# Kernel optimization log

Hardware: AMD Instinct MI355X
Metric: run time of the kernel (lower is better)

Reference implementation:

```python
import jax, jax.numpy as jnp
import numpy as np

B = 512      # batch (len(missing_type))
HALF = 12    # prompt_length // 3
D = 12       # prompt_depth
DT = 512     # text embed dim
DI = 768     # image embed dim
E = DT + DI  # 1280, concat dim
R = 16
H = E // R    # 80
HC = DT // R  # 32
EPS = 1e-5


def _ln(x, g, b):
    m = jnp.mean(x, -1, keepdims=True)
    v = jnp.mean((x - m) ** 2, -1, keepdims=True)
    return (x - m) * jax.lax.rsqrt(v + EPS) * g + b


def _mlp(x, w1, b1, w2, b2):
    return jax.nn.gelu(x @ w1 + b1, approximate=False) @ w2 + b2


def setup_inputs() -> dict:
    key = jax.random.key(0)
    ks = jax.random.split(key, 20)
    n = lambda k, s: jax.random.normal(k, s, dtype=jnp.float32) * 0.02
    return {
        "missing_type": jax.random.randint(ks[0], (B,), 0, 3),
        "vpc": n(ks[1], (HALF, DI)), "vpm": n(ks[2], (HALF, DI)),
        "tpc": n(ks[3], (HALF, DT)), "tpm": n(ks[4], (HALF, DT)),
        "cpc": n(ks[5], (HALF, DT)), "cpi": n(ks[6], (HALF, DT)), "cpt": n(ks[7], (HALF, DT)),
        "ln_img_g": jnp.ones((D, E)), "ln_img_b": jnp.zeros((D, E)),
        "ln_txt_g": jnp.ones((D, E)), "ln_txt_b": jnp.zeros((D, E)),
        "img_w1": n(ks[8], (D, E, H)), "img_b1": jnp.zeros((D, H)),
        "img_w2": n(ks[9], (D, H, DI)), "img_b2": jnp.zeros((D, DI)),
        "txt_w1": n(ks[10], (D, E, H)), "txt_b1": jnp.zeros((D, H)),
        "txt_w2": n(ks[11], (D, H, DT)), "txt_b2": jnp.zeros((D, DT)),
        "cimg_w1": n(ks[12], (DT, HC)), "cimg_b1": jnp.zeros((HC,)),
        "cimg_w2": n(ks[13], (HC, DI)), "cimg_b2": jnp.zeros((DI,)),
        "ctxt_w1": n(ks[14], (DT, HC)), "ctxt_b1": jnp.zeros((HC,)),
        "ctxt_w2": n(ks[15], (HC, DT)), "ctxt_b2": jnp.zeros((DT,)),
    }


def reference(missing_type, vpc, vpm, tpc, tpm, cpc, cpi, cpt,
              ln_img_g, ln_img_b, ln_txt_g, ln_txt_b,
              img_w1, img_b1, img_w2, img_b2,
              txt_w1, txt_b1, txt_w2, txt_b2,
              cimg_w1, cimg_b1, cimg_w2, cimg_b2,
              ctxt_w1, ctxt_b1, ctxt_w2, ctxt_b2):
    depth = img_w1.shape[0]
    mt = missing_type
    # per-sample branch selection, vectorized over the batch
    img = jnp.where((mt == 2)[:, None, None], vpm[None], vpc[None])  # [B,HALF,768]
    txt = jnp.where((mt == 1)[:, None, None], tpm[None], tpc[None])  # [B,HALF,512]
    common = jnp.stack([cpc, cpi, cpt])[mt]                          # [B,HALF,512]
    imgs, txts = [], []
    for d in range(depth):  # sequential depth dependency
        x = jnp.concatenate([img, txt], -1)  # [B,HALF,1280]
        img = _mlp(_ln(x, ln_img_g[d], ln_img_b[d]), img_w1[d], img_b1[d], img_w2[d], img_b2[d])
        txt = _mlp(_ln(x, ln_txt_g[d], ln_txt_b[d]), txt_w1[d], txt_b1[d], txt_w2[d], txt_b2[d])
        imgs.append(img)
        txts.append(txt)
    # depth-0 prompts get the projected common prompt appended along tokens
    img0 = jnp.concatenate([imgs[0], _mlp(common, cimg_w1, cimg_b1, cimg_w2, cimg_b2)], axis=1)
    txt0 = jnp.concatenate([txts[0], _mlp(common, ctxt_w1, ctxt_b1, ctxt_w2, ctxt_b2)], axis=1)
    return (img0, txt0, jnp.stack(imgs[1:]), jnp.stack(txts[1:]))
```

## Files before the change

kernel.cpp:

```cpp
#include <hip/hip_runtime.h>

typedef unsigned int u32;
typedef unsigned short u16;

#define TPB 640

namespace {
constexpr size_t F_WP1  = 0;
constexpr size_t F_WP2  = 1228800;
constexpr size_t F_XI_P = 1843200;
constexpr size_t F_XT_P = 2174976;
constexpr size_t F_CI_P = 2396160;
constexpr size_t F_CT_P = 2423808;
constexpr size_t F_END_P = 2442240;
constexpr size_t F_XI_U = 0;
constexpr size_t F_XT_U = 331776;
constexpr size_t F_CI_U = 552960;
constexpr size_t F_CT_U = 580608;
}

__device__ __forceinline__ float bflo(u32 u) { return __uint_as_float(u << 16); }
__device__ __forceinline__ float bfhi(u32 u) { return __uint_as_float(u & 0xffff0000u); }
__device__ __forceinline__ float gelu_f(float x) { return 0.5f * x * (1.0f + erff(x * 0.70710678118654752f)); }
__device__ __forceinline__ u16 f2bf(float f) {
    u32 u = __float_as_uint(f);
    u += 0x7fffu + ((u >> 16) & 1u);
    return (u16)(u >> 16);
}

struct P {
    const float *vpc, *vpm, *tpc, *tpm, *cpc, *cpi, *cpt;
    const float *lig, *lib, *ltg, *ltb;
    const float *iw1, *ib1, *iw2, *ib2;
    const float *tw1, *tb1, *tw2, *tb2;
    const float *ciw1, *cib1, *ciw2, *cib2;
    const float *ctw1, *ctb1, *ctw2, *ctb2;
    const u16 *wp1, *wp2;
    float *xi, *xt, *cimg, *ctxt;
};

__global__ __launch_bounds__(256) void prep_kernel(P p, u32* wp1o, u32* wp2o) {
    constexpr u32 N1 = 12u * 1280 * 80;
    constexpr u32 N2 = 12u * 80 * 640;
    u32 i = blockIdx.x * 256 + threadIdx.x;
    if (i < N1) {
        u32 j2 = i % 80, rem = i / 80;
        u32 k = rem % 1280, d = rem / 1280;
        u32 j0 = 2 * j2;
        const float* s = (j0 < 80) ? (p.iw1 + ((size_t)(d * 1280) + k) * 80 + j0)
                                   : (p.tw1 + ((size_t)(d * 1280) + k) * 80 + (j0 - 80));
        float2 v = *reinterpret_cast<const float2*>(s);
        wp1o[i] = (u32)f2bf(v.x) | ((u32)f2bf(v.y) << 16);
    } else {
        u32 ii = i - N1;
        if (ii >= N2) return;
        u32 c2 = ii % 640, rem = ii / 640;
        u32 k = rem % 80, d = rem / 80;
        u32 c0 = 2 * c2;
        const float* s = (c0 < 768) ? (p.iw2 + ((size_t)(d * 80) + k) * 768 + c0)
                                    : (p.tw2 + ((size_t)(d * 80) + k) * 512 + (c0 - 768));
        float2 v = *reinterpret_cast<const float2*>(s);
        wp2o[ii] = (u32)f2bf(v.x) | ((u32)f2bf(v.y) << 16);
    }
}

template <int PACKED>
__global__ __launch_bounds__(TPB) void chain_kernel(P p) {
    __shared__ float smem[6592];
    float* sx   = smem;
    float* xln0 = smem + 1280;
    float* xln1 = smem + 2560;
    float* part = smem + 3840;
    float* hh   = smem + 6400;
    float* redA = smem + 6560;
    float* redB = smem + 6570;
    float* st   = smem + 6580;

    const int tid = threadIdx.x;
    const int blk = blockIdx.x;

    if (blk < 36) {
        const int v = blk / 12, t = blk % 12;
        const float* is = (v == 2) ? p.vpm : p.vpc;
        const float* ts = (v == 1) ? p.tpm : p.tpc;
        if (tid < 512) { sx[768 + tid] = ts[t * 512 + tid]; }
        for (int k = tid; k < 768; k += TPB) sx[k] = is[t * 768 + k];
        __syncthreads();

        for (int d = 0; d < 12; ++d) {
            {
                float x0 = sx[tid], x1 = sx[tid + 640];
                float s = x0 + x1, s2 = x0 * x0 + x1 * x1;
                #pragma unroll
                for (int off = 32; off > 0; off >>= 1) { s += __shfl_down(s, off); s2 += __shfl_down(s2, off); }
                if ((tid & 63) == 0) { redA[tid >> 6] = s; redB[tid >> 6] = s2; }
            }
            __syncthreads();
            if (tid == 0) {
                float S = 0.f, S2 = 0.f;
                #pragma unroll
                for (int w = 0; w < 10; ++w) { S += redA[w]; S2 += redB[w]; }
                float m = S * (1.0f / 1280.0f);
                float var = S2 * (1.0f / 1280.0f) - m * m;
                st[0] = m; st[1] = rsqrtf(var + 1e-5f);
            }
            __syncthreads();
            const float m = st[0], rs = st[1];
            #pragma unroll
            for (int q = 0; q < 2; ++q) {
                const int k = tid + 640 * q;
                float xc = (sx[k] - m) * rs;
                xln0[k] = xc * p.lig[d * 1280 + k] + p.lib[d * 1280 + k];
                xln1[k] = xc * p.ltg[d * 1280 + k] + p.ltb[d * 1280 + k];
            }
            __syncthreads();
            {
                const int g = tid % 40, kc = tid / 40;
                const int j0 = 4 * g;
                const float* xl = (j0 >= 80) ? xln1 : xln0;
                const int k0 = kc * 80;
                float a0 = 0.f, a1 = 0.f, a2 = 0.f, a3 = 0.f;
                if (PACKED) {
                    const u16* wp = p.wp1 + ((size_t)(d * 1280) + k0) * 160 + j0;
                    #pragma unroll 16
                    for (int i = 0; i < 80; ++i) {
                        uint2 w = *reinterpret_cast<const uint2*>(wp);
                        float xv = xl[k0 + i];
                        a0 += xv * bflo(w.x); a1 += xv * bfhi(w.x);
                        a2 += xv * bflo(w.y); a3 += xv * bfhi(w.y);
                        wp += 160;
                    }
                } else {
                    const float* wp = (j0 < 80) ? (p.iw1 + ((size_t)(d * 1280) + k0) * 80 + j0)
                                                : (p.tw1 + ((size_t)(d * 1280) + k0) * 80 + (j0 - 80));
                    #pragma unroll 8
                    for (int i = 0; i < 80; ++i) {
                        float4 w = *reinterpret_cast<const float4*>(wp);
                        float xv = xl[k0 + i];
                        a0 += xv * w.x; a1 += xv * w.y; a2 += xv * w.z; a3 += xv * w.w;
                        wp += 80;
                    }
                }
                *reinterpret_cast<float4*>(part + kc * 160 + j0) = make_float4(a0, a1, a2, a3);
            }
            __syncthreads();
            if (tid < 160) {
                const int path = tid >= 80, j = tid - 80 * path;
                float a = (path ? p.tb1 : p.ib1)[d * 80 + j];
                #pragma unroll
                for (int kc = 0; kc < 16; ++kc) a += part[kc * 160 + tid];
                hh[tid] = gelu_f(a);
            }
            __syncthreads();
            {
                const int c = tid;
                const int pth = (c >= 384);
                const int cc = 2 * c - 768 * pth;
                const float* hb = hh + 80 * pth;
                float a0, a1;
                {
                    const float* b2 = (pth ? p.tb2 : p.ib2) + d * (pth ? 512 : 768) + cc;
                    a0 = b2[0]; a1 = b2[1];
                }
                if (PACKED) {
                    const u16* wp = p.wp2 + (size_t)(d * 80) * 1280 + 2 * c;
                    #pragma unroll 16
                    for (int k = 0; k < 80; ++k) {
                        u32 w = *reinterpret_cast<const u32*>(wp);
                        float hv = hb[k];
                        a0 += hv * bflo(w); a1 += hv * bfhi(w);
                        wp += 1280;
                    }
                } else {
                    const int Np = pth ? 512 : 768;
                    const float* wp = (pth ? p.tw2 + (size_t)(d * 80) * 512 : p.iw2 + (size_t)(d * 80) * 768) + cc;
                    #pragma unroll 16
                    for (int k = 0; k < 80; ++k) {
                        float2 w = *reinterpret_cast<const float2*>(wp);
                        float hv = hb[k];
                        a0 += hv * w.x; a1 += hv * w.y;
                        wp += Np;
                    }
                }
                sx[2 * c] = a0; sx[2 * c + 1] = a1;
                float* xo = pth ? (p.xt + ((size_t)(d * 36) + blk) * 512 + cc)
                                : (p.xi + ((size_t)(d * 36) + blk) * 768 + cc);
                *reinterpret_cast<float2*>(xo) = make_float2(a0, a1);
            }
            __syncthreads();
        }
    } else {
        float* cx  = smem;
        float* ph  = smem + 512;
        float* hhl = smem + 768;
        const int rr = blk - 36, v = rr / 12, t = rr % 12;
        const float* cs = (v == 0) ? p.cpc : (v == 1) ? p.cpi : p.cpt;
        if (tid < 512) cx[tid] = cs[t * 512 + tid];
        __syncthreads();
        if (tid < 256) {
            const int o = tid & 63, kc = tid >> 6;
            const int path = o >> 5, j = o & 31;
            const float* w = (path ? p.ctw1 : p.ciw1) + (size_t)(kc * 128) * 32 + j;
            float a = 0.f;
            #pragma unroll 8
            for (int i = 0; i < 128; ++i) { a += cx[kc * 128 + i] * (*w); w += 32; }
            ph[kc * 64 + o] = a;
        }
        __syncthreads();
        if (tid < 64) {
            const int path = tid >> 5, j = tid & 31;
            float a = (path ? p.ctb1 : p.cib1)[j];
            #pragma unroll
            for (int kc = 0; kc < 4; ++kc) a += ph[kc * 64 + tid];
            hhl[tid] = gelu_f(a);
        }
        __syncthreads();
        for (int o = tid; o < 1280; o += TPB) {
            if (o < 768) {
                float a = p.cib2[o];
                #pragma unroll
                for (int k = 0; k < 32; ++k) a += hhl[k] * p.ciw2[k * 768 + o];
                p.cimg[rr * 768 + o] = a;
            } else {
                const int oo = o - 768;
                float a = p.ctb2[oo];
                #pragma unroll
                for (int k = 0; k < 32; ++k) a += hhl[32 + k] * p.ctw2[k * 512 + oo];
                p.ctxt[rr * 512 + oo] = a;
            }
        }
    }
}

__global__ __launch_bounds__(256) void emit_kernel(const int* __restrict__ mt,
                                                   const float* __restrict__ xi,
                                                   const float* __restrict__ xt,
                                                   const float* __restrict__ cimg,
                                                   const float* __restrict__ ctxt,
                                                   float* __restrict__ out) {
    constexpr unsigned int C0 = 512u * 24 * 192;
    constexpr unsigned int C1 = 512u * 24 * 128;
    constexpr unsigned int C2 = 11u * 512 * 12 * 192;
    constexpr unsigned int C3 = 11u * 512 * 12 * 128;
    constexpr unsigned int TOT = C0 + C1 + C2 + C3;
    const unsigned int stride = gridDim.x * blockDim.x;
    for (unsigned int c = blockIdx.x * blockDim.x + threadIdx.x; c < TOT; c += stride) {
        const float* src;
        if (c < C0) {
            unsigned int b = c / 4608u, r = c % 4608u;
            unsigned int tok = r / 192u, col = (r % 192u) * 4u;
            int v = mt[b];
            src = (tok < 12u) ? xi + ((size_t)v * 12 + tok) * 768 + col
                              : cimg + ((size_t)v * 12 + (tok - 12u)) * 768 + col;
        } else if (c < C0 + C1) {
            unsigned int cc = c - C0;
            unsigned int b = cc / 3072u, r = cc % 3072u;
            unsigned int tok = r / 128u, col = (r % 128u) * 4u;
            int v = mt[b];
            src = (tok < 12u) ? xt + ((size_t)v * 12 + tok) * 512 + col
                              : ctxt + ((size_t)v * 12 + (tok - 12u)) * 512 + col;
        } else if (c < C0 + C1 + C2) {
            unsigned int cc = c - C0 - C1;
            unsigned int d = cc / 1179648u, r = cc % 1179648u;
            unsigned int b = r / 2304u, rr = r % 2304u;
            unsigned int tok = rr / 192u, col = (rr % 192u) * 4u;
            int v = mt[b];
            src = xi + ((size_t)(d + 1) * 36 + v * 12 + tok) * 768 + col;
        } else {
            unsigned int cc = c - C0 - C1 - C2;
            unsigned int d = cc / 786432u, r = cc % 786432u;
            unsigned int b = r / 1536u, rr = r % 1536u;
            unsigned int tok = rr / 128u, col = (rr % 128u) * 4u;
            int v = mt[b];
            src = xt + ((size_t)(d + 1) * 36 + v * 12 + tok) * 512 + col;
        }
        *reinterpret_cast<float4*>(out + (size_t)c * 4) = *reinterpret_cast<const float4*>(src);
    }
}

extern "C" void kernel_launch(void* const* d_in, const int* in_sizes, int n_in,
                              void* d_out, int out_size, void* d_ws, size_t ws_size,
                              hipStream_t stream) {
    const int* mt = (const int*)d_in[0];
    float* ws = (float*)d_ws;
    P p;
    p.vpc  = (const float*)d_in[1];
    p.vpm  = (const float*)d_in[2];
    p.tpc  = (const float*)d_in[3];
    p.tpm  = (const float*)d_in[4];
    p.cpc  = (const float*)d_in[5];
    p.cpi  = (const float*)d_in[6];
    p.cpt  = (const float*)d_in[7];
    p.lig  = (const float*)d_in[8];
    p.lib  = (const float*)d_in[9];
    p.ltg  = (const float*)d_in[10];
    p.ltb  = (const float*)d_in[11];
    p.iw1  = (const float*)d_in[12];
    p.ib1  = (const float*)d_in[13];
    p.iw2  = (const float*)d_in[14];
    p.ib2  = (const float*)d_in[15];
    p.tw1  = (const float*)d_in[16];
    p.tb1  = (const float*)d_in[17];
    p.tw2  = (const float*)d_in[18];
    p.tb2  = (const float*)d_in[19];
    p.ciw1 = (const float*)d_in[20];
    p.cib1 = (const float*)d_in[21];
    p.ciw2 = (const float*)d_in[22];
    p.cib2 = (const float*)d_in[23];
    p.ctw1 = (const float*)d_in[24];
    p.ctb1 = (const float*)d_in[25];
    p.ctw2 = (const float*)d_in[26];
    p.ctb2 = (const float*)d_in[27];

    const bool packed = (ws_size >= F_END_P * sizeof(float));
    if (packed) {
        p.wp1  = (const u16*)(ws + F_WP1);
        p.wp2  = (const u16*)(ws + F_WP2);
        p.xi   = ws + F_XI_P;
        p.xt   = ws + F_XT_P;
        p.cimg = ws + F_CI_P;
        p.ctxt = ws + F_CT_P;
        constexpr u32 NPAIR = 12u * 1280 * 80 + 12u * 80 * 640;
        prep_kernel<<<dim3((NPAIR + 255) / 256), dim3(256), 0, stream>>>(p, (u32*)(ws + F_WP1), (u32*)(ws + F_WP2));
        chain_kernel<1><<<dim3(72), dim3(TPB), 0, stream>>>(p);
    } else {
        p.wp1 = nullptr; p.wp2 = nullptr;
        p.xi   = ws + F_XI_U;
        p.xt   = ws + F_XT_U;
        p.cimg = ws + F_CI_U;
        p.ctxt = ws + F_CT_U;
        chain_kernel<0><<<dim3(72), dim3(TPB), 0, stream>>>(p);
    }
    emit_kernel<<<dim3(4096), dim3(256), 0, stream>>>(mt, p.xi, p.xt, p.cimg, p.ctxt, (float*)d_out);
}
```

Before: 216.1 us.

## Fold LayerNorm affine into packed first-layer weights and split K for second GEMV

The prep kernel now folds the LayerNorm gamma into the bf16 first-layer weights and precomputes per-column sums (s1) and bias-folded offsets (t1). The chain kernel can then run the first GEMV directly on the raw activations and apply mean and rstd afterwards, which removes the normalized-activation pass and one barrier. The first GEMV now reads 8 outputs per thread with wider loads, and the second GEMV is split over two K-chunks so all 640 threads work on it. The cost is an extra reduction step and a slower prep kernel that loops serially over K. The algebraic rewrite can also lose precision when the mean is large.

```diff
diff --git a/kernel.cpp b/kernel.cpp
--- a/kernel.cpp
+++ b/kernel.cpp
@@ -8,11 +8,13 @@
 namespace {
 constexpr size_t F_WP1  = 0;
 constexpr size_t F_WP2  = 1228800;
-constexpr size_t F_XI_P = 1843200;
-constexpr size_t F_XT_P = 2174976;
-constexpr size_t F_CI_P = 2396160;
-constexpr size_t F_CT_P = 2423808;
-constexpr size_t F_END_P = 2442240;
+constexpr size_t F_S1   = 1843200;
+constexpr size_t F_T1   = 1845120;
+constexpr size_t F_XI_P = 1847040;
+constexpr size_t F_XT_P = 2178816;
+constexpr size_t F_CI_P = 2400000;
+constexpr size_t F_CT_P = 2427648;
+constexpr size_t F_END_P = 2446080;
 constexpr size_t F_XI_U = 0;
 constexpr size_t F_XT_U = 331776;
 constexpr size_t F_CI_U = 552960;
@@ -36,36 +38,191 @@
     const float *ciw1, *cib1, *ciw2, *cib2;
     const float *ctw1, *ctb1, *ctw2, *ctb2;
     const u16 *wp1, *wp2;
+    const float *s1, *t1;
     float *xi, *xt, *cimg, *ctxt;
 };
 
-__global__ __launch_bounds__(256) void prep_kernel(P p, u32* wp1o, u32* wp2o) {
-    constexpr u32 N1 = 12u * 1280 * 80;
-    constexpr u32 N2 = 12u * 80 * 640;
-    u32 i = blockIdx.x * 256 + threadIdx.x;
-    if (i < N1) {
-        u32 j2 = i % 80, rem = i / 80;
-        u32 k = rem % 1280, d = rem / 1280;
-        u32 j0 = 2 * j2;
-        const float* s = (j0 < 80) ? (p.iw1 + ((size_t)(d * 1280) + k) * 80 + j0)
-                                   : (p.tw1 + ((size_t)(d * 1280) + k) * 80 + (j0 - 80));
-        float2 v = *reinterpret_cast<const float2*>(s);
-        wp1o[i] = (u32)f2bf(v.x) | ((u32)f2bf(v.y) << 16);
+__global__ __launch_bounds__(320) void prep_kernel(P p, u16* wp1o, u32* wp2o, float* s1o, float* t1o) {
+    __shared__ float sA[4][80], sB[4][80];
+    const int t = threadIdx.x;
+    if (blockIdx.x < 24) {
+        const int d = blockIdx.x >> 1, path = blockIdx.x & 1;
+        const float* W1 = (path ? p.tw1 : p.iw1) + (size_t)d * 1280 * 80;
+        const float* G  = (path ? p.ltg : p.lig) + d * 1280;
+        const float* Bb = (path ? p.ltb : p.lib) + d * 1280;
+        const int j = t % 80, kc = t / 80;
+        float S = 0.f, T = 0.f;
+        for (int k = kc * 320; k < kc * 320 + 320; ++k) {
+            float w = W1[(size_t)k * 80 + j];
+            float wg = G[k] * w;
+            S += wg; T += Bb[k] * w;
+            wp1o[((size_t)(d * 1280) + k) * 160 + path * 80 + j] = f2bf(wg);
+        }
+        sA[kc][j] = S; sB[kc][j] = T;
+        __syncthreads();
+        if (t < 80) {
+            float Ssum = sA[0][t] + sA[1][t] + sA[2][t] + sA[3][t];
+            float Tsum = sB[0][t] + sB[1][t] + sB[2][t] + sB[3][t];
+            s1o[d * 160 + path * 80 + t] = Ssum;
+            t1o[d * 160 + path * 80 + t] = Tsum + (path ? p.tb1 : p.ib1)[d * 80 + t];
+        }
     } else {
-        u32 ii = i - N1;
-        if (ii >= N2) return;
-        u32 c2 = ii % 640, rem = ii / 640;
+        constexpr u32 N2 = 12u * 80 * 640;
+        u32 i = (blockIdx.x - 24) * 320 + t;
+        if (i >= N2) return;
+        u32 c2 = i % 640, rem = i / 640;
         u32 k = rem % 80, d = rem / 80;
         u32 c0 = 2 * c2;
         const float* s = (c0 < 768) ? (p.iw2 + ((size_t)(d * 80) + k) * 768 + c0)
                                     : (p.tw2 + ((size_t)(d * 80) + k) * 512 + (c0 - 768));
         float2 v = *reinterpret_cast<const float2*>(s);
-        wp2o[ii] = (u32)f2bf(v.x) | ((u32)f2bf(v.y) << 16);
+        wp2o[i] = (u32)f2bf(v.x) | ((u32)f2bf(v.y) << 16);
     }
 }
 
-template <int PACKED>
-__global__ __launch_bounds__(TPB) void chain_kernel(P p) {
+__global__ __launch_bounds__(TPB) void chain2_kernel(P p) {
+    __shared__ float smem[6608];
+    float* sx   = smem;
+    float* part = smem + 1280;
+    float* hh   = smem + 6400;
+    float* redA = smem + 6560;
+    float* redB = smem + 6580;
+    float* st   = smem + 6600;
+
+    const int tid = threadIdx.x;
+    const int blk = blockIdx.x;
+
+    if (blk < 36) {
+        const int v = blk / 12, t = blk % 12;
+        const float* is = (v == 2) ? p.vpm : p.vpc;
+        const float* ts = (v == 1) ? p.tpm : p.tpc;
+        for (int k = tid; k < 768; k += TPB) sx[k] = is[t * 768 + k];
+        if (tid < 512) sx[768 + tid] = ts[t * 512 + tid];
+        __syncthreads();
+
+        for (int d = 0; d < 12; ++d) {
+            {
+                float x0 = sx[tid], x1 = sx[tid + 640];
+                float s = x0 + x1, s2 = x0 * x0 + x1 * x1;
+                #pragma unroll
+                for (int off = 32; off > 0; off >>= 1) { s += __shfl_down(s, off); s2 += __shfl_down(s2, off); }
+                if ((tid & 63) == 0) { redA[tid >> 6] = s; redB[tid >> 6] = s2; }
+            }
+            __syncthreads();
+            if (tid == 0) {
+                float S = 0.f, S2 = 0.f;
+                #pragma unroll
+                for (int w = 0; w < 10; ++w) { S += redA[w]; S2 += redB[w]; }
+                float m = S * (1.0f / 1280.0f);
+                float var = S2 * (1.0f / 1280.0f) - m * m;
+                st[0] = m; st[1] = rsqrtf(var + 1e-5f);
+            }
+            {
+                const int g = tid % 20, kc = tid / 20;
+                const int j0 = 8 * g, k0 = 40 * kc;
+                const u16* wp = p.wp1 + ((size_t)(d * 1280) + k0) * 160 + j0;
+                float a0 = 0.f, a1 = 0.f, a2 = 0.f, a3 = 0.f;
+                float a4 = 0.f, a5 = 0.f, a6 = 0.f, a7 = 0.f;
+                #pragma unroll 8
+                for (int i = 0; i < 40; ++i) {
+                    uint4 w = *reinterpret_cast<const uint4*>(wp);
+                    float xv = sx[k0 + i];
+                    a0 += xv * bflo(w.x); a1 += xv * bfhi(w.x);
+                    a2 += xv * bflo(w.y); a3 += xv * bfhi(w.y);
+                    a4 += xv * bflo(w.z); a5 += xv * bfhi(w.z);
+                    a6 += xv * bflo(w.w); a7 += xv * bfhi(w.w);
+                    wp += 160;
+                }
+                *reinterpret_cast<float4*>(part + kc * 160 + j0)     = make_float4(a0, a1, a2, a3);
+                *reinterpret_cast<float4*>(part + kc * 160 + j0 + 4) = make_float4(a4, a5, a6, a7);
+            }
+            __syncthreads();
+            if (tid < 160) {
+                float y = 0.f;
+                #pragma unroll
+                for (int kc = 0; kc < 32; ++kc) y += part[kc * 160 + tid];
+                const float m = st[0], rs = st[1];
+                float hpre = rs * y - m * rs * p.s1[d * 160 + tid] + p.t1[d * 160 + tid];
+                hh[tid] = gelu_f(hpre);
+            }
+            __syncthreads();
+            {
+                const int g2 = tid % 320, kc = tid / 320;
+                const int c0 = 4 * g2, k0 = 40 * kc;
+                const u16* wq = p.wp2 + ((size_t)(d * 80) + k0) * 1280 + c0;
+                const float* hb = hh + ((c0 >= 768) ? 80 : 0);
+                float a0 = 0.f, a1 = 0.f, a2 = 0.f, a3 = 0.f;
+                #pragma unroll 8
+                for (int i = 0; i < 40; ++i) {
+                    uint2 w = *reinterpret_cast<const uint2*>(wq);
+                    float hv = hb[k0 + i];
+                    a0 += hv * bflo(w.x); a1 += hv * bfhi(w.x);
+                    a2 += hv * bflo(w.y); a3 += hv * bfhi(w.y);
+                    wq += 1280;
+                }
+                *reinterpret_cast<float4*>(part + kc * 1280 + c0) = make_float4(a0, a1, a2, a3);
+            }
+            __syncthreads();
+            {
+                const int c0 = 2 * tid;
+                const int pth = (c0 >= 768);
+                const int cc = c0 - 768 * pth;
+                const int Np = pth ? 512 : 768;
+                float2 bb = *reinterpret_cast<const float2*>((pth ? p.tb2 : p.ib2) + d * Np + cc);
+                float a0 = part[c0]     + part[1280 + c0]     + bb.x;
+                float a1 = part[c0 + 1] + part[1280 + c0 + 1] + bb.y;
+                __syncthreads();
+                sx[c0] = a0; sx[c0 + 1] = a1;
+                float* xo = pth ? (p.xt + ((size_t)(d * 36) + blk) * 512 + cc)
+                                : (p.xi + ((size_t)(d * 36) + blk) * 768 + cc);
+                *reinterpret_cast<float2*>(xo) = make_float2(a0, a1);
+            }
+            __syncthreads();
+        }
+    } else {
+        float* cx  = smem;
+        float* ph  = smem + 512;
+        float* hhl = smem + 768;
+        const int rr = blk - 36, v = rr / 12, t = rr % 12;
+        const float* cs = (v == 0) ? p.cpc : (v == 1) ? p.cpi : p.cpt;
+        if (tid < 512) cx[tid] = cs[t * 512 + tid];
+        __syncthreads();
+        if (tid < 256) {
+            const int o = tid & 63, kc = tid >> 6;
+            const int path = o >> 5, j = o & 31;
+            const float* w = (path ? p.ctw1 : p.ciw1) + (size_t)(kc * 128) * 32 + j;
+            float a = 0.f;
+            #pragma unroll 8
+            for (int i = 0; i < 128; ++i) { a += cx[kc * 128 + i] * (*w); w += 32; }
+            ph[kc * 64 + o] = a;
+        }
+        __syncthreads();
+        if (tid < 64) {
+            const int path = tid >> 5, j = tid & 31;
+            float a = (path ? p.ctb1 : p.cib1)[j];
+            #pragma unroll
+            for (int kc = 0; kc < 4; ++kc) a += ph[kc * 64 + tid];
+            hhl[tid] = gelu_f(a);
+        }
+        __syncthreads();
+        for (int o = tid; o < 1280; o += TPB) {
+            if (o < 768) {
+                float a = p.cib2[o];
+                #pragma unroll
+                for (int k = 0; k < 32; ++k) a += hhl[k] * p.ciw2[k * 768 + o];
+                p.cimg[rr * 768 + o] = a;
+            } else {
+                const int oo = o - 768;
+                float a = p.ctb2[oo];
+                #pragma unroll
+                for (int k = 0; k < 32; ++k) a += hhl[32 + k] * p.ctw2[k * 512 + oo];
+                p.ctxt[rr * 512 + oo] = a;
+            }
+        }
+    }
+}
+
+__global__ __launch_bounds__(TPB) void chain_fb_kernel(P p) {
     __shared__ float smem[6592];
     float* sx   = smem;
     float* xln0 = smem + 1280;
@@ -83,10 +240,9 @@
         const int v = blk / 12, t = blk % 12;
         const float* is = (v == 2) ? p.vpm : p.vpc;
         const float* ts = (v == 1) ? p.tpm : p.tpc;
-        if (tid < 512) { sx[768 + tid] = ts[t * 512 + tid]; }
+        if (tid < 512) sx[768 + tid] = ts[t * 512 + tid];
         for (int k = tid; k < 768; k += TPB) sx[k] = is[t * 768 + k];
         __syncthreads();
-
         for (int d = 0; d < 12; ++d) {
             {
                 float x0 = sx[tid], x1 = sx[tid + 640];
@@ -120,26 +276,14 @@
                 const float* xl = (j0 >= 80) ? xln1 : xln0;
                 const int k0 = kc * 80;
                 float a0 = 0.f, a1 = 0.f, a2 = 0.f, a3 = 0.f;
-                if (PACKED) {
-                    const u16* wp = p.wp1 + ((size_t)(d * 1280) + k0) * 160 + j0;
-                    #pragma unroll 16
-                    for (int i = 0; i < 80; ++i) {
-                        uint2 w = *reinterpret_cast<const uint2*>(wp);
-                        float xv = xl[k0 + i];
-                        a0 += xv * bflo(w.x); a1 += xv * bfhi(w.x);
-                        a2 += xv * bflo(w.y); a3 += xv * bfhi(w.y);
-                        wp += 160;
-                    }
-                } else {
-                    const float* wp = (j0 < 80) ? (p.iw1 + ((size_t)(d * 1280) + k0) * 80 + j0)
-                                                : (p.tw1 + ((size_t)(d * 1280) + k0) * 80 + (j0 - 80));
-                    #pragma unroll 8
-                    for (int i = 0; i < 80; ++i) {
-                        float4 w = *reinterpret_cast<const float4*>(wp);
-                        float xv = xl[k0 + i];
-                        a0 += xv * w.x; a1 += xv * w.y; a2 += xv * w.z; a3 += xv * w.w;
-                        wp += 80;
-                    }
+                const float* wp = (j0 < 80) ? (p.iw1 + ((size_t)(d * 1280) + k0) * 80 + j0)
+                                            : (p.tw1 + ((size_t)(d * 1280) + k0) * 80 + (j0 - 80));
+                #pragma unroll 8
+                for (int i = 0; i < 80; ++i) {
+                    float4 w = *reinterpret_cast<const float4*>(wp);
+                    float xv = xl[k0 + i];
+                    a0 += xv * w.x; a1 += xv * w.y; a2 += xv * w.z; a3 += xv * w.w;
+                    wp += 80;
                 }
                 *reinterpret_cast<float4*>(part + kc * 160 + j0) = make_float4(a0, a1, a2, a3);
             }
@@ -157,30 +301,16 @@
                 const int pth = (c >= 384);
                 const int cc = 2 * c - 768 * pth;
                 const float* hb = hh + 80 * pth;
-                float a0, a1;
-                {
-                    const float* b2 = (pth ? p.tb2 : p.ib2) + d * (pth ? 512 : 768) + cc;
-                    a0 = b2[0]; a1 = b2[1];
-                }
-                if (PACKED) {
-                    const u16* wp = p.wp2 + (size_t)(d * 80) * 1280 + 2 * c;
-                    #pragma unroll 16
-                    for (int k = 0; k < 80; ++k) {
-                        u32 w = *reinterpret_cast<const u32*>(wp);
-                        float hv = hb[k];
-                        a0 += hv * bflo(w); a1 += hv * bfhi(w);
-                        wp += 1280;
-                    }
-                } else {
-                    const int Np = pth ? 512 : 768;
-                    const float* wp = (pth ? p.tw2 + (size_t)(d * 80) * 512 : p.iw2 + (size_t)(d * 80) * 768) + cc;
-                    #pragma unroll 16
-                    for (int k = 0; k < 80; ++k) {
-                        float2 w = *reinterpret_cast<const float2*>(wp);
-                        float hv = hb[k];
-                        a0 += hv * w.x; a1 += hv * w.y;
-                        wp += Np;
-                    }
+                const int Np = pth ? 512 : 768;
+                const float* b2 = (pth ? p.tb2 : p.ib2) + d * Np + cc;
+                float a0 = b2[0], a1 = b2[1];
+                const float* wp = (pth ? p.tw2 + (size_t)(d * 80) * 512 : p.iw2 + (size_t)(d * 80) * 768) + cc;
+                #pragma unroll 16
+                for (int k = 0; k < 80; ++k) {
+                    float2 w = *reinterpret_cast<const float2*>(wp);
+                    float hv = hb[k];
+                    a0 += hv * w.x; a1 += hv * w.y;
+                    wp += Np;
                 }
                 sx[2 * c] = a0; sx[2 * c + 1] = a1;
                 float* xo = pth ? (p.xt + ((size_t)(d * 36) + blk) * 512 + cc)
@@ -316,20 +446,24 @@
     if (packed) {
         p.wp1  = (const u16*)(ws + F_WP1);
         p.wp2  = (const u16*)(ws + F_WP2);
+        p.s1   = ws + F_S1;
+        p.t1   = ws + F_T1;
         p.xi   = ws + F_XI_P;
         p.xt   = ws + F_XT_P;
         p.cimg = ws + F_CI_P;
         p.ctxt = ws + F_CT_P;
-        constexpr u32 NPAIR = 12u * 1280 * 80 + 12u * 80 * 640;
-        prep_kernel<<<dim3((NPAIR + 255) / 256), dim3(256), 0, stream>>>(p, (u32*)(ws + F_WP1), (u32*)(ws + F_WP2));
-        chain_kernel<1><<<dim3(72), dim3(TPB), 0, stream>>>(p);
+        constexpr u32 N2 = 12u * 80 * 640;
+        const int nb = 24 + (N2 + 319) / 320;
+        prep_kernel<<<dim3(nb), dim3(320), 0, stream>>>(p, (u16*)(ws + F_WP1), (u32*)(ws + F_WP2),
+                                                        ws + F_S1, ws + F_T1);
+        chain2_kernel<<<dim3(72), dim3(TPB), 0, stream>>>(p);
     } else {
-        p.wp1 = nullptr; p.wp2 = nullptr;
+        p.wp1 = nullptr; p.wp2 = nullptr; p.s1 = nullptr; p.t1 = nullptr;
         p.xi   = ws + F_XI_U;
         p.xt   = ws + F_XT_U;
         p.cimg = ws + F_CI_U;
         p.ctxt = ws + F_CT_U;
-        chain_kernel<0><<<dim3(72), dim3(TPB), 0, stream>>>(p);
+        chain_fb_kernel<<<dim3(72), dim3(TPB), 0, stream>>>(p);
     }
     emit_kernel<<<dim3(4096), dim3(256), 0, stream>>>(mt, p.xi, p.xt, p.cimg, p.ctxt, (float*)d_out);
 }
```

Result: slower. 268.4 us (+24.2%).
